# Optimization experiments

Hardware: AMD Instinct MI355X
Metric: run time of the kernel (lower is better)

## Reference

```python
import jax, jax.numpy as jnp
import numpy as np

N_NODES = 50000
N_EDGES = 800000
IN_FEAT = 256
OUT_FEAT = 256
NUM_RELS = 8
ALPHA = 0.5


def setup_inputs() -> dict:
    key = jax.random.key(0)
    k1, k2, k3, k4, k5, k6 = jax.random.split(key, 6)
    x = jax.random.normal(k1, (N_NODES, IN_FEAT), dtype=jnp.float32)
    edge_index = jax.random.randint(k2, (2, N_EDGES), 0, N_NODES, dtype=jnp.int64)
    edge_type = jax.random.randint(k3, (N_EDGES,), 0, NUM_RELS, dtype=jnp.int64)
    # Xavier-uniform-ish init for weights (scale per fan-in/fan-out)
    gain = float(np.sqrt(2.0))  # calculate_gain('relu')
    lim_w = gain * float(np.sqrt(6.0 / (IN_FEAT + OUT_FEAT)))
    weight = jax.random.uniform(k4, (NUM_RELS, IN_FEAT, OUT_FEAT), dtype=jnp.float32,
                                minval=-lim_w, maxval=lim_w)
    loop_weight = jax.random.uniform(k5, (IN_FEAT, OUT_FEAT), dtype=jnp.float32,
                                     minval=-lim_w, maxval=lim_w)
    h_bias = jnp.zeros((OUT_FEAT,), dtype=jnp.float32)
    return {"edge_index": edge_index, "x": x, "edge_type": edge_type,
            "weight": weight, "h_bias": h_bias, "loop_weight": loop_weight}


def reference(edge_index, x, edge_type, weight, h_bias, loop_weight):
    num_nodes = x.shape[0]
    src, dst = edge_index[0], edge_index[1]
    # Per-edge message msg_e = x[src_e] @ weight[edge_type_e].
    # Computed efficiently as num_rels dense GEMMs over all nodes, then a fused
    # (relation, src) gather — identical math, avoids (E, in, out) weight blowup.
    hx = jnp.einsum('ni,rio->rno', x, weight)          # (R, N, out)
    msg = hx[edge_type, src]                            # (E, out)
    agg = jax.ops.segment_sum(msg, dst, num_segments=num_nodes)  # (N, out)
    node_repr = agg * jnp.asarray(ALPHA, x.dtype) ** 0.5
    node_repr = node_repr + h_bias
    loop_message = x @ loop_weight                      # (N, out)
    node_repr = node_repr + loop_message * jnp.asarray(1.0 - ALPHA, x.dtype) ** 0.5
    # activation=None, dropout=0.0 (eval) -> identity
    return node_repr
```

## Files before the change

### kernel.cpp

```cpp
#include <hip/hip_runtime.h>

typedef __bf16 bf16x8 __attribute__((ext_vector_type(8)));
typedef float f32x4 __attribute__((ext_vector_type(4)));

static __device__ __forceinline__ unsigned short f2bf(float f) {
    unsigned u = __builtin_bit_cast(unsigned, f);
    u += 0x7FFFu + ((u >> 16) & 1u);
    return (unsigned short)(u >> 16);
}
static __device__ __forceinline__ float bf2f(unsigned short h) {
    return __builtin_bit_cast(float, ((unsigned)h) << 16);
}

#define GLOAD_LDS16(g, l)                                              \
    __builtin_amdgcn_global_load_lds(                                  \
        (const __attribute__((address_space(1))) unsigned int*)(g),    \
        (__attribute__((address_space(3))) unsigned int*)(l), 16, 0, 0)

__global__ __launch_bounds__(256) void rgcn_zero(unsigned* __restrict__ p, int n) {
    int i = blockIdx.x * 256 + threadIdx.x;
    if (i < n) p[i] = 0;
}

__global__ __launch_bounds__(256) void rgcn_hist(const int* __restrict__ ei,
                                                 unsigned* __restrict__ cnt, int E) {
    int e = blockIdx.x * 256 + threadIdx.x;
    if (e < E) atomicAdd(&cnt[ei[E + e]], 1u);
}

__global__ __launch_bounds__(1024) void rgcn_scan1(const unsigned* __restrict__ cnt,
                                                   unsigned* __restrict__ off,
                                                   unsigned* __restrict__ bsum, int n) {
    __shared__ unsigned ws[16];
    const int t = threadIdx.x, lane = t & 63, wv = t >> 6;
    int i = blockIdx.x * 1024 + t;
    unsigned v = (i < n) ? cnt[i] : 0;
    unsigned s = v;
    #pragma unroll
    for (int d = 1; d < 64; d <<= 1) {
        unsigned u = __shfl_up(s, d, 64);
        if (lane >= d) s += u;
    }
    if (lane == 63) ws[wv] = s;
    __syncthreads();
    if (wv == 0) {
        unsigned b = (lane < 16) ? ws[lane] : 0;
        unsigned sb = b;
        #pragma unroll
        for (int d = 1; d < 16; d <<= 1) {
            unsigned u = __shfl_up(sb, d, 64);
            if (lane >= d) sb += u;
        }
        if (lane < 16) ws[lane] = sb - b;
        if (lane == 15) bsum[blockIdx.x] = sb;
    }
    __syncthreads();
    if (i < n) off[i] = ws[wv] + (s - v);
}

__global__ __launch_bounds__(64) void rgcn_scan2(unsigned* __restrict__ bsum,
                                                 unsigned* __restrict__ bsumo,
                                                 unsigned* __restrict__ off, int nb, int n) {
    const int lane = threadIdx.x & 63;
    unsigned b = (lane < nb) ? bsum[lane] : 0;
    unsigned s = b;
    #pragma unroll
    for (int d = 1; d < 64; d <<= 1) {
        unsigned u = __shfl_up(s, d, 64);
        if (lane >= d) s += u;
    }
    if (lane < nb) bsumo[lane] = s - b;
    if (lane == 63) off[n] = s;
}

__global__ __launch_bounds__(256) void rgcn_scan3(unsigned* __restrict__ off,
                                                  const unsigned* __restrict__ bsumo,
                                                  unsigned* __restrict__ cur, int n) {
    int i = blockIdx.x * 256 + threadIdx.x;
    if (i < n) {
        unsigned v = off[i] + bsumo[i >> 10];
        off[i] = v;
        cur[i] = v;
    }
}

__global__ __launch_bounds__(256) void rgcn_scatter(const int* __restrict__ ei,
                                                    const int* __restrict__ et,
                                                    unsigned* __restrict__ cur,
                                                    unsigned* __restrict__ recs, int E) {
    int e = blockIdx.x * 256 + threadIdx.x;
    if (e < E) {
        int dst = ei[E + e];
        unsigned p = atomicAdd(&cur[dst], 1u);
        recs[p] = (unsigned)ei[e] | ((unsigned)et[e] << 16);
    }
}

__global__ __launch_bounds__(256) void rgcn_cvt(const float* __restrict__ x,
                                                unsigned short* __restrict__ Z, int M) {
    int w = (blockIdx.x * 256 + threadIdx.x) >> 6;
    int lane = threadIdx.x & 63;
    if (w >= M) return;
    float4 v = *(const float4*)(x + (size_t)w * 256 + lane * 4);
    ushort4 o;
    o.x = f2bf(v.x); o.y = f2bf(v.y); o.z = f2bf(v.z); o.w = f2bf(v.w);
    *(ushort4*)(Z + (size_t)w * 2304 + 2048 + lane * 4) = o;
}

__global__ __launch_bounds__(256) void rgcn_wbt(const float* __restrict__ w,
                                                const float* __restrict__ lw,
                                                unsigned short* __restrict__ wbT) {
    int kc = blockIdx.x * 256 + threadIdx.x;
    int n  = blockIdx.y;
    if (kc >= 2304) return;
    float v;
    if (kc < 2048) {
        int r = kc >> 8, k = kc & 255;
        v = w[((size_t)r * 256 + k) * 256 + n];
    } else {
        v = lw[(size_t)(kc - 2048) * 256 + n];
    }
    wbT[(size_t)n * 2304 + kc] = f2bf(v * 0.70710678118654752f);
}

__global__ __launch_bounds__(256) void rgcn_agg(const unsigned* __restrict__ recs,
                                                const unsigned* __restrict__ off,
                                                unsigned short* __restrict__ Z, int M) {
    const int gw0  = (blockIdx.x * 256 + threadIdx.x) >> 6;
    const int nw   = (gridDim.x * 256) >> 6;
    const int lane = threadIdx.x & 63;

#define LOADF(rec, fv)                                                                 \
    {                                                                                  \
        const ushort4 v_ = *(const ushort4*)(Z + (size_t)((rec) & 0xFFFFu) * 2304 +    \
                                             2048 + lane * 4);                         \
        fv[0] = bf2f(v_.x); fv[1] = bf2f(v_.y); fv[2] = bf2f(v_.z); fv[3] = bf2f(v_.w);\
    }
#define ACCUM(rec, fv)                                                                 \
    switch ((rec) >> 16) {                                                             \
        case 0: a0 += fv; break; case 1: a1 += fv; break;                              \
        case 2: a2 += fv; break; case 3: a3 += fv; break;                              \
        case 4: a4 += fv; break; case 5: a5 += fv; break;                              \
        case 6: a6 += fv; break; default: a7 += fv; break;                             \
    }

    for (int w = gw0; w < M; w += nw) {
        unsigned o0 = off[w], o1 = off[w + 1];
        f32x4 a0 = {}, a1 = {}, a2 = {}, a3 = {}, a4 = {}, a5 = {}, a6 = {}, a7 = {};

        unsigned i = o0;
        for (; i + 8 <= o1; i += 8) {
            unsigned r0 = recs[i],     r1 = recs[i + 1], r2 = recs[i + 2], r3 = recs[i + 3];
            unsigned r4 = recs[i + 4], r5 = recs[i + 5], r6 = recs[i + 6], r7 = recs[i + 7];
            f32x4 f0, f1, f2, f3, f4, f5, f6, f7;
            LOADF(r0, f0); LOADF(r1, f1); LOADF(r2, f2); LOADF(r3, f3);
            LOADF(r4, f4); LOADF(r5, f5); LOADF(r6, f6); LOADF(r7, f7);
            ACCUM(r0, f0); ACCUM(r1, f1); ACCUM(r2, f2); ACCUM(r3, f3);
            ACCUM(r4, f4); ACCUM(r5, f5); ACCUM(r6, f6); ACCUM(r7, f7);
        }
        for (; i < o1; ++i) {
            unsigned r0 = recs[i];
            f32x4 f0;
            LOADF(r0, f0);
            ACCUM(r0, f0);
        }

        unsigned short* zr = Z + (size_t)w * 2304 + lane * 4;
#define ST(rr, ax)                                                                     \
        {                                                                              \
            ushort4 o_;                                                                \
            o_.x = f2bf(ax[0]); o_.y = f2bf(ax[1]);                                    \
            o_.z = f2bf(ax[2]); o_.w = f2bf(ax[3]);                                    \
            *(ushort4*)(zr + rr * 256) = o_;                                           \
        }
        ST(0, a0) ST(1, a1) ST(2, a2) ST(3, a3) ST(4, a4) ST(5, a5) ST(6, a6) ST(7, a7)
#undef ST
    }
#undef LOADF
#undef ACCUM
}

#define BM 64
#define BK 64
#define NCH 36

__global__ __launch_bounds__(256) void rgcn_gemm(
    const unsigned short* __restrict__ A,
    const unsigned short* __restrict__ Bt,
    float* __restrict__ out,
    const float* __restrict__ bias,
    int M)
{
    __shared__ char lds[8192 * 2 + 32768];
    char* Ab0 = lds;
    char* Ab1 = lds + 8192;
    char* Bb  = lds + 16384;

    const int tid  = threadIdx.x;
    const int lane = tid & 63;
    const int wid  = tid >> 6;
    const int wn   = wid * 64;
    const int m0   = blockIdx.x * BM;

    f32x4 acc[4][4] = {};

    auto stageA = [&](int chunk, char* dst) {
        #pragma unroll
        for (int it = 0; it < 2; ++it) {
            int o   = it * 4096 + tid * 16;
            int r   = o >> 7;
            int scb = (o & 127) ^ ((r & 7) << 4);
            int ga  = m0 + r; if (ga >= M) ga = M - 1;
            GLOAD_LDS16((const char*)A + (size_t)ga * 4608 + (size_t)chunk * 128 + scb, dst + o);
        }
    };
    auto stageB = [&](int chunk) {
        #pragma unroll
        for (int it = 0; it < 8; ++it) {
            int o   = it * 4096 + tid * 16;
            int r   = o >> 7;
            int scb = (o & 127) ^ ((r & 7) << 4);
            GLOAD_LDS16((const char*)Bt + (size_t)r * 4608 + (size_t)chunk * 128 + scb, Bb + o);
        }
    };

    stageA(0, Ab0);
    stageB(0);
    stageA(1, Ab1);
    asm volatile("s_waitcnt vmcnt(2)" ::: "memory");
    __builtin_amdgcn_s_barrier();
    __builtin_amdgcn_sched_barrier(0);

    for (int t = 0; t < NCH; ++t) {
        const char* Acur = (t & 1) ? Ab1 : Ab0;
        #pragma unroll
        for (int kk = 0; kk < 2; ++kk) {
            const int koff = kk * 32 + (lane >> 4) * 8;
            bf16x8 af[4], bfr[4];
            #pragma unroll
            for (int i = 0; i < 4; ++i) {
                int ar = i * 16 + (lane & 15);
                af[i] = *(const bf16x8*)(Acur + ((ar * 128 + koff * 2) ^ ((ar & 7) << 4)));
            }
            #pragma unroll
            for (int j = 0; j < 4; ++j) {
                int br = wn + j * 16 + (lane & 15);
                bfr[j] = *(const bf16x8*)(Bb + ((br * 128 + koff * 2) ^ ((br & 7) << 4)));
            }
            #pragma unroll
            for (int i = 0; i < 4; ++i)
                #pragma unroll
                for (int j = 0; j < 4; ++j)
                    acc[i][j] = __builtin_amdgcn_mfma_f32_16x16x32_bf16(af[i], bfr[j], acc[i][j], 0, 0, 0);
        }

        if (t < NCH - 1) {
            __builtin_amdgcn_s_barrier();
            __builtin_amdgcn_sched_barrier(0);
            stageB(t + 1);
            int tA = (t + 2 < NCH) ? t + 2 : NCH - 1;
            stageA(tA, (t & 1) ? Ab1 : Ab0);
            asm volatile("s_waitcnt vmcnt(2)" ::: "memory");
            __builtin_amdgcn_s_barrier();
            __builtin_amdgcn_sched_barrier(0);
        }
    }

    const int col = lane & 15;
    const int r0  = (lane >> 4) * 4;
    #pragma unroll
    for (int i = 0; i < 4; ++i) {
        #pragma unroll
        for (int j = 0; j < 4; ++j) {
            int gn = wn + j * 16 + col;
            float bv = bias[gn];
            #pragma unroll
            for (int rr = 0; rr < 4; ++rr) {
                int gm = m0 + i * 16 + r0 + rr;
                if (gm < M) out[(size_t)gm * 256 + gn] = acc[i][j][rr] + bv;
            }
        }
    }
}

extern "C" void kernel_launch(void* const* d_in, const int* in_sizes, int n_in,
                              void* d_out, int out_size, void* d_ws, size_t ws_size,
                              hipStream_t stream) {
    const int*   edge_index = (const int*)d_in[0];
    const float* x          = (const float*)d_in[1];
    const int*   edge_type  = (const int*)d_in[2];
    const float* weight     = (const float*)d_in[3];
    const float* h_bias     = (const float*)d_in[4];
    const float* loop_w     = (const float*)d_in[5];
    float* out = (float*)d_out;

    const int M = in_sizes[1] / 256;
    const int E = in_sizes[2];

    char* ws = (char*)d_ws;
    size_t off_b = 0;
    unsigned short* Zcat = (unsigned short*)(ws + off_b);
    off_b += (((size_t)M * 2304 * 2) + 255) & ~(size_t)255;
    unsigned short* wbT = (unsigned short*)(ws + off_b);
    off_b += (((size_t)256 * 2304 * 2) + 255) & ~(size_t)255;
    unsigned* cnt = (unsigned*)(ws + off_b);
    off_b += (((size_t)(M + 1) * 4) + 255) & ~(size_t)255;
    unsigned* off = (unsigned*)(ws + off_b);
    off_b += (((size_t)(M + 1) * 4) + 255) & ~(size_t)255;
    unsigned* bsum = (unsigned*)(ws + off_b);
    off_b += 256;
    unsigned* bsumo = (unsigned*)(ws + off_b);
    off_b += 256;
    unsigned* recs = (unsigned*)(ws + off_b);

    const int nb = (M + 1023) / 1024;

    rgcn_zero<<<(M + 255) / 256, 256, 0, stream>>>(cnt, M);
    rgcn_hist<<<(E + 255) / 256, 256, 0, stream>>>(edge_index, cnt, E);
    rgcn_scan1<<<nb, 1024, 0, stream>>>(cnt, off, bsum, M);
    rgcn_scan2<<<1, 64, 0, stream>>>(bsum, bsumo, off, nb, M);
    rgcn_scan3<<<(M + 255) / 256, 256, 0, stream>>>(off, bsumo, cnt, M);
    rgcn_scatter<<<(E + 255) / 256, 256, 0, stream>>>(edge_index, edge_type, cnt, recs, E);

    rgcn_cvt<<<(M + 3) / 4, 256, 0, stream>>>(x, Zcat, M);
    rgcn_wbt<<<dim3(9, 256), 256, 0, stream>>>(weight, loop_w, wbT);

    rgcn_agg<<<2560, 256, 0, stream>>>(recs, off, Zcat, M);

    rgcn_gemm<<<(M + BM - 1) / BM, 256, 0, stream>>>(Zcat, wbT, out, h_bias, M);
}
```

Measured before the change: 343.9 us.

## Fuse histogram/convert/weight-transpose kernels and cooperatively load edge records in aggregation

Merges the destination histogram, x-to-bf16 conversion and weight transpose into one launch with block-range dispatch, removing two kernel launches and letting the independent work overlap. The aggregation kernel now loads up to 64 edge records at once with one coalesced load per lane and broadcasts them with shuffles, then issues 16 gathers at a time, instead of each lane redundantly reading the same records. This is meant to cut redundant record loads and raise memory-level parallelism, at the cost of more registers for the 16-wide unroll.

```diff
diff --git a/kernel.cpp b/kernel.cpp
--- a/kernel.cpp
+++ b/kernel.cpp
@@ -22,10 +22,43 @@
     if (i < n) p[i] = 0;
 }
 
-__global__ __launch_bounds__(256) void rgcn_hist(const int* __restrict__ ei,
-                                                 unsigned* __restrict__ cnt, int E) {
-    int e = blockIdx.x * 256 + threadIdx.x;
-    if (e < E) atomicAdd(&cnt[ei[E + e]], 1u);
+__global__ __launch_bounds__(256) void rgcn_prep(const int* __restrict__ ei,
+                                                 unsigned* __restrict__ cnt,
+                                                 const float* __restrict__ x,
+                                                 unsigned short* __restrict__ Z,
+                                                 const float* __restrict__ w,
+                                                 const float* __restrict__ lw,
+                                                 unsigned short* __restrict__ wbT,
+                                                 int E, int M, int HB, int CB) {
+    const int b = blockIdx.x;
+    const int t = threadIdx.x;
+    if (b < HB) {
+        int e = b * 256 + t;
+        if (e < E) atomicAdd(&cnt[ei[E + e]], 1u);
+    } else if (b < HB + CB) {
+        int wv = ((b - HB) * 256 + t) >> 6;
+        int lane = t & 63;
+        if (wv < M) {
+            float4 v = *(const float4*)(x + (size_t)wv * 256 + lane * 4);
+            ushort4 o;
+            o.x = f2bf(v.x); o.y = f2bf(v.y); o.z = f2bf(v.z); o.w = f2bf(v.w);
+            *(ushort4*)(Z + (size_t)wv * 2304 + 2048 + lane * 4) = o;
+        }
+    } else {
+        int bb = b - HB - CB;
+        int kc = (bb % 9) * 256 + t;
+        int n  = bb / 9;
+        if (kc < 2304) {
+            float v;
+            if (kc < 2048) {
+                int r = kc >> 8, k = kc & 255;
+                v = w[((size_t)r * 256 + k) * 256 + n];
+            } else {
+                v = lw[(size_t)(kc - 2048) * 256 + n];
+            }
+            wbT[(size_t)n * 2304 + kc] = f2bf(v * 0.70710678118654752f);
+        }
+    }
 }
 
 __global__ __launch_bounds__(1024) void rgcn_scan1(const unsigned* __restrict__ cnt,
@@ -96,87 +129,75 @@
     }
 }
 
-__global__ __launch_bounds__(256) void rgcn_cvt(const float* __restrict__ x,
-                                                unsigned short* __restrict__ Z, int M) {
-    int w = (blockIdx.x * 256 + threadIdx.x) >> 6;
-    int lane = threadIdx.x & 63;
-    if (w >= M) return;
-    float4 v = *(const float4*)(x + (size_t)w * 256 + lane * 4);
-    ushort4 o;
-    o.x = f2bf(v.x); o.y = f2bf(v.y); o.z = f2bf(v.z); o.w = f2bf(v.w);
-    *(ushort4*)(Z + (size_t)w * 2304 + 2048 + lane * 4) = o;
-}
-
-__global__ __launch_bounds__(256) void rgcn_wbt(const float* __restrict__ w,
-                                                const float* __restrict__ lw,
-                                                unsigned short* __restrict__ wbT) {
-    int kc = blockIdx.x * 256 + threadIdx.x;
-    int n  = blockIdx.y;
-    if (kc >= 2304) return;
-    float v;
-    if (kc < 2048) {
-        int r = kc >> 8, k = kc & 255;
-        v = w[((size_t)r * 256 + k) * 256 + n];
-    } else {
-        v = lw[(size_t)(kc - 2048) * 256 + n];
-    }
-    wbT[(size_t)n * 2304 + kc] = f2bf(v * 0.70710678118654752f);
-}
-
 __global__ __launch_bounds__(256) void rgcn_agg(const unsigned* __restrict__ recs,
                                                 const unsigned* __restrict__ off,
                                                 unsigned short* __restrict__ Z, int M) {
     const int gw0  = (blockIdx.x * 256 + threadIdx.x) >> 6;
     const int nw   = (gridDim.x * 256) >> 6;
     const int lane = threadIdx.x & 63;
-
-#define LOADF(rec, fv)                                                                 \
+    const unsigned short* Zx = Z + 2048 + lane * 4;
+
+#define GATHER(rr) (*(const ushort4*)(Zx + (size_t)((rr) & 0xFFFFu) * 2304))
+#define ACCUM(rec, v_)                                                                 \
     {                                                                                  \
-        const ushort4 v_ = *(const ushort4*)(Z + (size_t)((rec) & 0xFFFFu) * 2304 +    \
-                                             2048 + lane * 4);                         \
+        f32x4 fv;                                                                      \
         fv[0] = bf2f(v_.x); fv[1] = bf2f(v_.y); fv[2] = bf2f(v_.z); fv[3] = bf2f(v_.w);\
-    }
-#define ACCUM(rec, fv)                                                                 \
-    switch ((rec) >> 16) {                                                             \
-        case 0: a0 += fv; break; case 1: a1 += fv; break;                              \
-        case 2: a2 += fv; break; case 3: a3 += fv; break;                              \
-        case 4: a4 += fv; break; case 5: a5 += fv; break;                              \
-        case 6: a6 += fv; break; default: a7 += fv; break;                             \
+        switch ((rec) >> 16) {                                                         \
+            case 0: a0 += fv; break; case 1: a1 += fv; break;                          \
+            case 2: a2 += fv; break; case 3: a3 += fv; break;                          \
+            case 4: a4 += fv; break; case 5: a5 += fv; break;                          \
+            case 6: a6 += fv; break; default: a7 += fv; break;                         \
+        }                                                                              \
     }
 
     for (int w = gw0; w < M; w += nw) {
-        unsigned o0 = off[w], o1 = off[w + 1];
+        const unsigned o0 = off[w], o1 = off[w + 1];
         f32x4 a0 = {}, a1 = {}, a2 = {}, a3 = {}, a4 = {}, a5 = {}, a6 = {}, a7 = {};
 
-        unsigned i = o0;
-        for (; i + 8 <= o1; i += 8) {
-            unsigned r0 = recs[i],     r1 = recs[i + 1], r2 = recs[i + 2], r3 = recs[i + 3];
-            unsigned r4 = recs[i + 4], r5 = recs[i + 5], r6 = recs[i + 6], r7 = recs[i + 7];
-            f32x4 f0, f1, f2, f3, f4, f5, f6, f7;
-            LOADF(r0, f0); LOADF(r1, f1); LOADF(r2, f2); LOADF(r3, f3);
-            LOADF(r4, f4); LOADF(r5, f5); LOADF(r6, f6); LOADF(r7, f7);
-            ACCUM(r0, f0); ACCUM(r1, f1); ACCUM(r2, f2); ACCUM(r3, f3);
-            ACCUM(r4, f4); ACCUM(r5, f5); ACCUM(r6, f6); ACCUM(r7, f7);
-        }
-        for (; i < o1; ++i) {
-            unsigned r0 = recs[i];
-            f32x4 f0;
-            LOADF(r0, f0);
-            ACCUM(r0, f0);
+        for (unsigned base = o0; base < o1; base += 64) {
+            const unsigned wdeg = (o1 - base < 64u) ? (o1 - base) : 64u;
+            const unsigned myrec = ((unsigned)lane < wdeg) ? recs[base + lane] : 0u;
+
+            unsigned j = 0;
+            for (; j + 16 <= wdeg; j += 16) {
+                unsigned rr[16];
+                #pragma unroll
+                for (int u = 0; u < 16; ++u) rr[u] = __shfl(myrec, (int)(j + u), 64);
+                ushort4 vv[16];
+                #pragma unroll
+                for (int u = 0; u < 16; ++u) vv[u] = GATHER(rr[u]);
+                #pragma unroll
+                for (int u = 0; u < 16; ++u) ACCUM(rr[u], vv[u]);
+            }
+            for (; j + 4 <= wdeg; j += 4) {
+                unsigned rr[4];
+                #pragma unroll
+                for (int u = 0; u < 4; ++u) rr[u] = __shfl(myrec, (int)(j + u), 64);
+                ushort4 vv[4];
+                #pragma unroll
+                for (int u = 0; u < 4; ++u) vv[u] = GATHER(rr[u]);
+                #pragma unroll
+                for (int u = 0; u < 4; ++u) ACCUM(rr[u], vv[u]);
+            }
+            for (; j < wdeg; ++j) {
+                unsigned r_ = __shfl(myrec, (int)j, 64);
+                ushort4 v_ = GATHER(r_);
+                ACCUM(r_, v_);
+            }
         }
 
         unsigned short* zr = Z + (size_t)w * 2304 + lane * 4;
-#define ST(rr, ax)                                                                     \
+#define ST(rr_, ax)                                                                    \
         {                                                                              \
             ushort4 o_;                                                                \
             o_.x = f2bf(ax[0]); o_.y = f2bf(ax[1]);                                    \
             o_.z = f2bf(ax[2]); o_.w = f2bf(ax[3]);                                    \
-            *(ushort4*)(zr + rr * 256) = o_;                                           \
+            *(ushort4*)(zr + rr_ * 256) = o_;                                          \
         }
         ST(0, a0) ST(1, a1) ST(2, a2) ST(3, a3) ST(4, a4) ST(5, a5) ST(6, a6) ST(7, a7)
 #undef ST
     }
-#undef LOADF
+#undef GATHER
 #undef ACCUM
 }
 
@@ -314,17 +335,17 @@
     unsigned* recs = (unsigned*)(ws + off_b);
 
     const int nb = (M + 1023) / 1024;
+    const int HB = (E + 255) / 256;
+    const int CB = (M + 3) / 4;
 
     rgcn_zero<<<(M + 255) / 256, 256, 0, stream>>>(cnt, M);
-    rgcn_hist<<<(E + 255) / 256, 256, 0, stream>>>(edge_index, cnt, E);
+    rgcn_prep<<<HB + CB + 2304, 256, 0, stream>>>(edge_index, cnt, x, Zcat,
+                                                  weight, loop_w, wbT, E, M, HB, CB);
     rgcn_scan1<<<nb, 1024, 0, stream>>>(cnt, off, bsum, M);
     rgcn_scan2<<<1, 64, 0, stream>>>(bsum, bsumo, off, nb, M);
     rgcn_scan3<<<(M + 255) / 256, 256, 0, stream>>>(off, bsumo, cnt, M);
     rgcn_scatter<<<(E + 255) / 256, 256, 0, stream>>>(edge_index, edge_type, cnt, recs, E);
 
-    rgcn_cvt<<<(M + 3) / 4, 256, 0, stream>>>(x, Zcat, M);
-    rgcn_wbt<<<dim3(9, 256), 256, 0, stream>>>(weight, loop_w, wbT);
-
     rgcn_agg<<<2560, 256, 0, stream>>>(recs, off, Zcat, M);
 
     rgcn_gemm<<<(M + BM - 1) / BM, 256, 0, stream>>>(Zcat, wbT, out, h_bias, M);
```

Result: faster. 333.1 us (-3.2%).
